# Kernel tuning notes

Measured on AMD Instinct MI355X. Metric: run time of the kernel, lower is better.

## Reference

```python
import jax, jax.numpy as jnp
import numpy as np

N_NODES = 8192
D = 7      # in_dim == out_dim (hardcoded 7x7 weight)
K = 32     # kNN fan-out


def setup_inputs() -> dict:
    key = jax.random.key(0)
    k1, k2, k3 = jax.random.split(key, 3)
    x = jax.random.normal(k1, (N_NODES, D + 1), dtype=jnp.float32)
    W = jax.random.normal(k2, (D, D), dtype=jnp.float32) * np.float32(1.0 / np.sqrt(D))
    a = jax.random.normal(k3, (2 * D,), dtype=jnp.float32) * np.float32(0.1)
    return {"x": x, "W": W, "a": a}


def _forward(x, W, a, k=K):
    # split pollutant channel (last column) from features, as in the torch forward
    pollutant = x[:, -1]          # (N,)
    feat = x[:, :-1]              # (N, D)
    N, d = feat.shape

    # linear transform (nn.functional.linear(x, weight) == x @ W.T)
    out = feat @ W.T              # (N, D)
    # nonlinearity_1 = Hardtanh
    out = jnp.clip(out, -1.0, 1.0)
    # (feature_weight = softmax(a) is computed in torch but unused for 'affine' kernel)

    # kNN graph built from input features (use_previous_graph=True).
    # Squared distances give the same neighbor ordering as euclidean norms.
    sq = jnp.sum(feat * feat, axis=1)                       # (N,)
    dist2 = sq[:, None] + sq[None, :] - 2.0 * (feat @ feat.T)
    dist2 = jnp.maximum(dist2, 0.0)
    dist2 = jnp.where(jnp.eye(N, dtype=bool), jnp.inf, dist2)  # dist[dist==0] = inf (self)
    _, nbr = jax.lax.top_k(-dist2, k)                       # (N, k) nearest neighbors

    out_n = out[nbr]                                        # (N, k, D) neighbor gather
    # affine attention: score_ij = concat(out_i, out_j) . a
    s = (out @ a[:d])[:, None] + out_n @ a[d:]              # (N, k)
    att = jax.nn.softmax(s, axis=-1)                        # per-node softmax over neighbors

    pol_n = pollutant[nbr]                                  # (N, k)
    xp = jnp.concatenate([out_n, pol_n[..., None]], axis=-1)  # (N, k, D+1)
    agg = jnp.einsum('nk,nkd->nd', att, xp)                 # attention-weighted aggregate

    y = jnp.concatenate([out, agg], axis=-1)                # (N, 2D+1)
    return y, att


def reference(x, W, a):
    y, att = _forward(x, W, a)
    # torch returns (y, y_, a) where y_ is y and a is the last node's attention row
    return (y, y, att[-1])
```

## Files before the change

### kernel.cpp

```cpp
#include <hip/hip_runtime.h>
#include <math.h>
#include <stdint.h>

#define N_NODES 8192
#define D 7
#define K 32
#define NT 512
#define QB 8
#define CPT (N_NODES / NT)
#define SUBC 8
#define ECAP2 256
#define DELTA 0.125f

typedef unsigned long long u64;
typedef _Float16 h2 __attribute__((ext_vector_type(2)));

__device__ __forceinline__ float rfl(float v) {
    return __uint_as_float(__builtin_amdgcn_readfirstlane(__float_as_uint(v)));
}
__device__ __forceinline__ unsigned rflu(unsigned v) {
    return __builtin_amdgcn_readfirstlane(v);
}
__device__ __forceinline__ h2 h2u(unsigned u) {
    union { unsigned u; h2 h; } t; t.u = u; return t.h;
}
__device__ __forceinline__ unsigned pkh(float a, float b) {
    union { h2 h; unsigned u; } t;
    t.h[0] = (_Float16)a; t.h[1] = (_Float16)b; return t.u;
}
__device__ __forceinline__ unsigned ordu(float f) {
    unsigned u = __float_as_uint(f);
    return (u & 0x80000000u) ? ~u : (u | 0x80000000u);
}
__device__ __forceinline__ float unordu(unsigned o) {
    unsigned u = (o & 0x80000000u) ? (o & 0x7fffffffu) : ~o;
    return __uint_as_float(u);
}

#if __has_builtin(__builtin_amdgcn_fdot2)
#define FDOT2(a, b, c) __builtin_amdgcn_fdot2((a), (b), (c), false)
#else
__device__ __forceinline__ float FDOT2(h2 a, h2 b, float c) {
    return fmaf((float)a[1], (float)b[1], fmaf((float)a[0], (float)b[0], c));
}
#endif

__device__ __forceinline__ float dist_m(float4 b0, float4 b1, float sqj,
                                        float4 A, float4 B) {
    float dot = A.x * b0.x;
    dot = fmaf(A.y, b0.y, dot);
    dot = fmaf(A.z, b0.z, dot);
    dot = fmaf(A.w, b0.w, dot);
    dot = fmaf(B.x, b1.x, dot);
    dot = fmaf(B.y, b1.y, dot);
    dot = fmaf(B.z, b1.z, dot);
    return fmaf(-2.0f, dot, sqj);
}

__device__ __forceinline__ float screen_m(uint4 dj, unsigned s0, unsigned s1,
                                          unsigned s2, unsigned s3) {
    return FDOT2(h2u(dj.x), h2u(s0),
           FDOT2(h2u(dj.y), h2u(s1),
           FDOT2(h2u(dj.z), h2u(s2),
           FDOT2(h2u(dj.w), h2u(s3), 0.f))));
}

__global__ __launch_bounds__(256)
void precompute_kernel(const float* __restrict__ x, const float* __restrict__ W,
                       float* __restrict__ outb, uint4* __restrict__ fh,
                       float4* __restrict__ xsq4)
{
    int n = blockIdx.x * 256 + threadIdx.x;
    float4 v0 = *reinterpret_cast<const float4*>(x + n * 8);
    float4 v1 = *reinterpret_cast<const float4*>(x + n * 8 + 4);
    float f[D] = {v0.x, v0.y, v0.z, v0.w, v1.x, v1.y, v1.z};
    float sq = 0.f;
#pragma unroll
    for (int c = 0; c < D; ++c) sq += f[c] * f[c];
    uint4 h;
    h.x = pkh(f[0], f[1]); h.y = pkh(f[2], f[3]);
    h.z = pkh(f[4], f[5]); h.w = pkh(f[6], sq);
    fh[n] = h;
    xsq4[n * 2]     = v0;
    xsq4[n * 2 + 1] = make_float4(v1.x, v1.y, v1.z, sq);
#pragma unroll
    for (int r = 0; r < D; ++r) {
        float acc = 0.f;
#pragma unroll
        for (int c = 0; c < D; ++c) acc += f[c] * W[r * D + c];
        acc = fminf(fmaxf(acc, -1.f), 1.f);
        outb[n * D + r] = acc;
    }
}

__global__ __launch_bounds__(NT, 4)
void gat_kernel(const float* __restrict__ x, const float* __restrict__ aw,
                const float* __restrict__ outb, const uint4* __restrict__ fh,
                const float4* __restrict__ xs4, float* __restrict__ dout)
{
    __shared__ u64      cand[QB][ECAP2];
    __shared__ int      nbr[QB][K];
    __shared__ unsigned selT[QB];
    __shared__ int      cnt2[QB];
    __shared__ float    redv[8];
    __shared__ int      redi[8];
    __shared__ float    bcv;
    __shared__ int      bci;

    float* Lmin = (float*)cand;

    const int tid  = threadIdx.x;
    const int lane = tid & 63;
    const int wave = tid >> 6;
    const int i0   = blockIdx.x * QB;

    unsigned qs0[QB], qs1[QB], qs2[QB], qs3[QB];
    float4 qA[QB], qBv[QB];
    float sqi[QB];
#pragma unroll
    for (int q = 0; q < QB; ++q) {
        const float* xq = x + (i0 + q) * 8;
        float4 a0 = *reinterpret_cast<const float4*>(xq);
        float4 a1 = *reinterpret_cast<const float4*>(xq + 4);
        float sq_ = rfl(xs4[(i0 + q) * 2 + 1].w);
        qs0[q] = rflu(pkh(-2.f * a0.x, -2.f * a0.y));
        qs1[q] = rflu(pkh(-2.f * a0.z, -2.f * a0.w));
        qs2[q] = rflu(pkh(-2.f * a1.x, -2.f * a1.y));
        qs3[q] = rflu(pkh(-2.f * a1.z, 1.0f));
        qA[q].x  = rfl(a0.x); qA[q].y  = rfl(a0.y);
        qA[q].z  = rfl(a0.z); qA[q].w  = rfl(a0.w);
        qBv[q].x = rfl(a1.x); qBv[q].y = rfl(a1.y);
        qBv[q].z = rfl(a1.z); qBv[q].w = sq_;
        sqi[q]   = sq_;
    }
    if (tid < QB) cnt2[tid] = 0;

    float lm[QB];
#pragma unroll
    for (int q = 0; q < QB; ++q) lm[q] = INFINITY;

#pragma unroll 4
    for (int c = 0; c < SUBC; ++c) {
        uint4 dj = fh[c * NT + tid];
#pragma unroll
        for (int q = 0; q < QB; ++q)
            lm[q] = fminf(lm[q], screen_m(dj, qs0[q], qs1[q], qs2[q], qs3[q]));
    }
#pragma unroll
    for (int q = 0; q < QB; ++q) Lmin[q * NT + tid] = lm[q];
    __syncthreads();

    {
        const int q = wave;
        unsigned ov0 = ordu(Lmin[q * NT +   0 + lane]);
        unsigned ov1 = ordu(Lmin[q * NT +  64 + lane]);
        unsigned ov2 = ordu(Lmin[q * NT + 128 + lane]);
        unsigned ov3 = ordu(Lmin[q * NT + 192 + lane]);
        unsigned ov4 = ordu(Lmin[q * NT + 256 + lane]);
        unsigned ov5 = ordu(Lmin[q * NT + 320 + lane]);
        unsigned ov6 = ordu(Lmin[q * NT + 384 + lane]);
        unsigned ov7 = ordu(Lmin[q * NT + 448 + lane]);
        unsigned lo = 0u, hi = 0xFFFFFFFFu;
        while (lo < hi) {
            unsigned mid = lo + ((hi - lo) >> 1);
            int cnt = __popcll(__ballot(ov0 <= mid))
                    + __popcll(__ballot(ov1 <= mid))
                    + __popcll(__ballot(ov2 <= mid))
                    + __popcll(__ballot(ov3 <= mid))
                    + __popcll(__ballot(ov4 <= mid))
                    + __popcll(__ballot(ov5 <= mid))
                    + __popcll(__ballot(ov6 <= mid))
                    + __popcll(__ballot(ov7 <= mid));
            if (cnt >= 34) hi = mid; else lo = mid + 1;
        }
        if (lane == 0) selT[q] = lo;
    }
    __syncthreads();

    float exq[QB];
#pragma unroll
    for (int q = 0; q < QB; ++q)
        exq[q] = fmaxf(unordu(selT[q]) + DELTA, -sqi[q]);

#pragma unroll 2
    for (int c = 0; c < CPT; ++c) {
        int j = c * NT + tid;
        float4 b0 = xs4[j * 2];
        float4 b1 = xs4[j * 2 + 1];
#pragma unroll
        for (int q = 0; q < QB; ++q) {
            float m = dist_m(b0, b1, b1.w, qA[q], qBv[q]);
            if (m <= exq[q] && j != i0 + q) {
                float d2c = fmaxf(sqi[q] + m, 0.f);
                u64 key = ((u64)__float_as_uint(d2c) << 32) | (unsigned)j;
                int p = atomicAdd(&cnt2[q], 1);
                if (p < ECAP2) cand[q][p] = key;
            }
        }
    }
    __syncthreads();

    {
        const int q = wave;
        const int M = cnt2[q];
        if (M >= K && M <= ECAP2) {
            for (int p = lane; p < M; p += 64) {
                u64 my = cand[q][p];
                int rank = 0;
                for (int m = 0; m < M; ++m)
                    rank += (cand[q][m] < my) ? 1 : 0;
                if (rank < K) nbr[q][rank] = (int)(my & 0xffffffffu);
            }
        }
    }
    __syncthreads();

#pragma unroll 1
    for (int q = 0; q < QB; ++q) {
        int M = cnt2[q];
        if (M < K || M > ECAP2) {
            const int iq = i0 + q;
            const float* xq = x + iq * 8;
            float4 A  = *reinterpret_cast<const float4*>(xq);
            float4 Bv = *reinterpret_cast<const float4*>(xq + 4);
            Bv.w = xs4[iq * 2 + 1].w;
            float lastv = -1.0f; int lasti = -1;
#pragma unroll 1
            for (int it = 0; it < K; ++it) {
                float best = INFINITY; int bidx = 0x7fffffff;
#pragma unroll 1
                for (int c = 0; c < CPT; ++c) {
                    int j = c * NT + tid;
                    float4 b0 = xs4[j * 2];
                    float4 b1 = xs4[j * 2 + 1];
                    float m = dist_m(b0, b1, b1.w, A, Bv);
                    float d2c = fmaxf(Bv.w + m, 0.f);
                    if (j == iq) continue;
                    bool gt = (d2c > lastv) || (d2c == lastv && j > lasti);
                    if (gt && (d2c < best || (d2c == best && j < bidx))) {
                        best = d2c; bidx = j;
                    }
                }
#pragma unroll
                for (int off = 32; off > 0; off >>= 1) {
                    float ov = __shfl_down(best, off);
                    int   oi = __shfl_down(bidx, off);
                    if (ov < best || (ov == best && oi < bidx)) { best = ov; bidx = oi; }
                }
                if (lane == 0) { redv[wave] = best; redi[wave] = bidx; }
                __syncthreads();
                if (tid == 0) {
                    float bv = redv[0]; int bi = redi[0];
#pragma unroll
                    for (int w = 1; w < 8; ++w)
                        if (redv[w] < bv || (redv[w] == bv && redi[w] < bi)) {
                            bv = redv[w]; bi = redi[w];
                        }
                    bcv = bv; bci = bi;
                    nbr[q][it] = bi;
                }
                __syncthreads();
                lastv = bcv; lasti = bci;
            }
        }
    }
    __syncthreads();

    {
        const int q  = wave;
        const int iq = i0 + q;
        if (lane < K) {
            int nk = nbr[q][lane];
            float s = 0.f;
#pragma unroll
            for (int c = 0; c < D; ++c) s += outb[iq * D + c] * aw[c];
            float xp[D + 1];
#pragma unroll
            for (int c = 0; c < D; ++c) {
                float on = outb[nk * D + c];
                xp[c] = on;
                s += on * aw[D + c];
            }
            xp[D] = x[nk * 8 + 7];

            float m = s;
#pragma unroll
            for (int off = 16; off > 0; off >>= 1) m = fmaxf(m, __shfl_xor(m, off, 32));
            float e = expf(s - m);
            float sum = e;
#pragma unroll
            for (int off = 16; off > 0; off >>= 1) sum += __shfl_xor(sum, off, 32);
            float att = e / sum;

            float agg[D + 1];
#pragma unroll
            for (int dd = 0; dd < D + 1; ++dd) {
                float v = att * xp[dd];
#pragma unroll
                for (int off = 16; off > 0; off >>= 1) v += __shfl_xor(v, off, 32);
                agg[dd] = v;
            }

            if (lane < D) {
                float o = outb[iq * D + lane];
                dout[iq * 15 + lane] = o;
                dout[N_NODES * 15 + iq * 15 + lane] = o;
            }
            if (lane < D + 1) {
                float av_ = agg[0];
#pragma unroll
                for (int dd = 1; dd < D + 1; ++dd) av_ = (lane == dd) ? agg[dd] : av_;
                dout[iq * 15 + D + lane] = av_;
                dout[N_NODES * 15 + iq * 15 + D + lane] = av_;
            }
            if (iq == N_NODES - 1) dout[2 * N_NODES * 15 + lane] = att;
        }
    }
}

extern "C" void kernel_launch(void* const* d_in, const int* in_sizes, int n_in,
                              void* d_out, int out_size, void* d_ws, size_t ws_size,
                              hipStream_t stream) {
    (void)in_sizes; (void)n_in; (void)out_size; (void)ws_size;
    const float* x = (const float*)d_in[0];
    const float* W = (const float*)d_in[1];
    const float* a = (const float*)d_in[2];
    float* out   = (float*)d_out;
    float* outb  = (float*)d_ws;
    uint4* fh    = (uint4*)(outb + N_NODES * D);
    float4* xsq4 = (float4*)(fh + N_NODES);

    hipLaunchKernelGGL(precompute_kernel, dim3(N_NODES / 256), dim3(256),
                       0, stream, x, W, outb, fh, xsq4);
    hipLaunchKernelGGL(gat_kernel, dim3(N_NODES / QB), dim3(NT),
                       0, stream, x, a, outb, fh, xsq4, out);
}
```

Measured before the change: 73.11 us.

## Use fp16 MFMA for kNN distance screening and a full-set candidate prefilter

Replaces the per-lane fdot2 screening over a subsample with 16x16x32 fp16 MFMA tiles over all nodes. The MFMA results feed both the per-tile minima used for threshold selection and a second screening pass that collects candidate indices into shared memory. The exact fp32 distance check then runs only on those candidates instead of scanning all 8192 nodes per query. This cuts the dense fp32 pass, but it adds a second full MFMA pass, shared-memory atomics, and fallback cases when the candidate list overflows.

```diff
diff --git a/kernel.cpp b/kernel.cpp
--- a/kernel.cpp
+++ b/kernel.cpp
@@ -8,21 +8,18 @@
 #define NT 512
 #define QB 8
 #define CPT (N_NODES / NT)
-#define SUBC 8
+#define SCAP 320
 #define ECAP2 256
 #define DELTA 0.125f
 
 typedef unsigned long long u64;
 typedef _Float16 h2 __attribute__((ext_vector_type(2)));
+typedef _Float16 f16x8 __attribute__((ext_vector_type(8)));
+typedef float f32x4 __attribute__((ext_vector_type(4)));
+union U4H8 { uint4 u; f16x8 h; };
 
 __device__ __forceinline__ float rfl(float v) {
     return __uint_as_float(__builtin_amdgcn_readfirstlane(__float_as_uint(v)));
-}
-__device__ __forceinline__ unsigned rflu(unsigned v) {
-    return __builtin_amdgcn_readfirstlane(v);
-}
-__device__ __forceinline__ h2 h2u(unsigned u) {
-    union { unsigned u; h2 h; } t; t.u = u; return t.h;
 }
 __device__ __forceinline__ unsigned pkh(float a, float b) {
     union { h2 h; unsigned u; } t;
@@ -36,14 +33,6 @@
     unsigned u = (o & 0x80000000u) ? (o & 0x7fffffffu) : ~o;
     return __uint_as_float(u);
 }
-
-#if __has_builtin(__builtin_amdgcn_fdot2)
-#define FDOT2(a, b, c) __builtin_amdgcn_fdot2((a), (b), (c), false)
-#else
-__device__ __forceinline__ float FDOT2(h2 a, h2 b, float c) {
-    return fmaf((float)a[1], (float)b[1], fmaf((float)a[0], (float)b[0], c));
-}
-#endif
 
 __device__ __forceinline__ float dist_m(float4 b0, float4 b1, float sqj,
                                         float4 A, float4 B) {
@@ -57,14 +46,6 @@
     return fmaf(-2.0f, dot, sqj);
 }
 
-__device__ __forceinline__ float screen_m(uint4 dj, unsigned s0, unsigned s1,
-                                          unsigned s2, unsigned s3) {
-    return FDOT2(h2u(dj.x), h2u(s0),
-           FDOT2(h2u(dj.y), h2u(s1),
-           FDOT2(h2u(dj.z), h2u(s2),
-           FDOT2(h2u(dj.w), h2u(s3), 0.f))));
-}
-
 __global__ __launch_bounds__(256)
 void precompute_kernel(const float* __restrict__ x, const float* __restrict__ W,
                        float* __restrict__ outb, uint4* __restrict__ fh,
@@ -99,8 +80,14 @@
                 const float4* __restrict__ xs4, float* __restrict__ dout)
 {
     __shared__ u64      cand[QB][ECAP2];
+    __shared__ unsigned short ent[QB][SCAP];
     __shared__ int      nbr[QB][K];
+    __shared__ uint4    qpk[16];
+    __shared__ float    sqfL[QB];
     __shared__ unsigned selT[QB];
+    __shared__ float    exqL[QB];
+    __shared__ float    scrL[16];
+    __shared__ int      scnt[QB];
     __shared__ int      cnt2[QB];
     __shared__ float    redv[8];
     __shared__ int      redi[8];
@@ -113,8 +100,9 @@
     const int lane = tid & 63;
     const int wave = tid >> 6;
     const int i0   = blockIdx.x * QB;
-
-    unsigned qs0[QB], qs1[QB], qs2[QB], qs3[QB];
+    const int col  = lane & 15;
+    const int lg   = lane >> 4;
+
     float4 qA[QB], qBv[QB];
     float sqi[QB];
 #pragma unroll
@@ -123,74 +111,116 @@
         float4 a0 = *reinterpret_cast<const float4*>(xq);
         float4 a1 = *reinterpret_cast<const float4*>(xq + 4);
         float sq_ = rfl(xs4[(i0 + q) * 2 + 1].w);
-        qs0[q] = rflu(pkh(-2.f * a0.x, -2.f * a0.y));
-        qs1[q] = rflu(pkh(-2.f * a0.z, -2.f * a0.w));
-        qs2[q] = rflu(pkh(-2.f * a1.x, -2.f * a1.y));
-        qs3[q] = rflu(pkh(-2.f * a1.z, 1.0f));
         qA[q].x  = rfl(a0.x); qA[q].y  = rfl(a0.y);
         qA[q].z  = rfl(a0.z); qA[q].w  = rfl(a0.w);
         qBv[q].x = rfl(a1.x); qBv[q].y = rfl(a1.y);
         qBv[q].z = rfl(a1.z); qBv[q].w = sq_;
         sqi[q]   = sq_;
     }
-    if (tid < QB) cnt2[tid] = 0;
-
-    float lm[QB];
-#pragma unroll
-    for (int q = 0; q < QB; ++q) lm[q] = INFINITY;
-
+    if (tid < 16) {
+        if (tid < QB) {
+            const float* xq = x + (i0 + tid) * 8;
+            float f0 = xq[0], f1 = xq[1], f2 = xq[2], f3 = xq[3];
+            float f4 = xq[4], f5 = xq[5], f6 = xq[6];
+            qpk[tid] = make_uint4(pkh(-2.f * f0, -2.f * f1),
+                                  pkh(-2.f * f2, -2.f * f3),
+                                  pkh(-2.f * f4, -2.f * f5),
+                                  pkh(-2.f * f6, 1.0f));
+            sqfL[tid] = f0*f0 + f1*f1 + f2*f2 + f3*f3 + f4*f4 + f5*f5 + f6*f6;
+            scnt[tid] = 0;
+            cnt2[tid] = 0;
+        } else {
+            qpk[tid] = make_uint4(0u, 0u, 0u, 0u);
+        }
+    }
+    __syncthreads();
+
+    U4H8 ub; ub.u = (lane < 16) ? qpk[lane] : make_uint4(0u, 0u, 0u, 0u);
+    const f16x8 bfrag = ub.h;
+    const f32x4 z4 = {0.f, 0.f, 0.f, 0.f};
+    const int tilebase = wave * 64;
+
+    float lm0 = INFINITY, lm1 = INFINITY, lm2 = INFINITY, lm3 = INFINITY;
 #pragma unroll 4
-    for (int c = 0; c < SUBC; ++c) {
-        uint4 dj = fh[c * NT + tid];
-#pragma unroll
-        for (int q = 0; q < QB; ++q)
-            lm[q] = fminf(lm[q], screen_m(dj, qs0[q], qs1[q], qs2[q], qs3[q]));
-    }
-#pragma unroll
-    for (int q = 0; q < QB; ++q) Lmin[q * NT + tid] = lm[q];
+    for (int tt = 0; tt < 64; ++tt) {
+        int t = tilebase + tt;
+        uint4 au = make_uint4(0u, 0u, 0u, 0u);
+        if (lane < 16) au = fh[t * 16 + lane];
+        U4H8 ua; ua.u = au;
+        f32x4 acc = __builtin_amdgcn_mfma_f32_16x16x32_f16(ua.h, bfrag, z4, 0, 0, 0);
+        lm0 = fminf(lm0, acc[0]);
+        lm1 = fminf(lm1, acc[1]);
+        lm2 = fminf(lm2, acc[2]);
+        lm3 = fminf(lm3, acc[3]);
+    }
+    {
+        int sb = wave * 16 + lg * 4;
+        Lmin[(sb + 0) * 16 + col] = lm0;
+        Lmin[(sb + 1) * 16 + col] = lm1;
+        Lmin[(sb + 2) * 16 + col] = lm2;
+        Lmin[(sb + 3) * 16 + col] = lm3;
+    }
     __syncthreads();
 
     {
         const int q = wave;
-        unsigned ov0 = ordu(Lmin[q * NT +   0 + lane]);
-        unsigned ov1 = ordu(Lmin[q * NT +  64 + lane]);
-        unsigned ov2 = ordu(Lmin[q * NT + 128 + lane]);
-        unsigned ov3 = ordu(Lmin[q * NT + 192 + lane]);
-        unsigned ov4 = ordu(Lmin[q * NT + 256 + lane]);
-        unsigned ov5 = ordu(Lmin[q * NT + 320 + lane]);
-        unsigned ov6 = ordu(Lmin[q * NT + 384 + lane]);
-        unsigned ov7 = ordu(Lmin[q * NT + 448 + lane]);
+        unsigned ov0 = ordu(Lmin[lane * 16 + q]);
+        unsigned ov1 = ordu(Lmin[(64 + lane) * 16 + q]);
         unsigned lo = 0u, hi = 0xFFFFFFFFu;
         while (lo < hi) {
             unsigned mid = lo + ((hi - lo) >> 1);
             int cnt = __popcll(__ballot(ov0 <= mid))
-                    + __popcll(__ballot(ov1 <= mid))
-                    + __popcll(__ballot(ov2 <= mid))
-                    + __popcll(__ballot(ov3 <= mid))
-                    + __popcll(__ballot(ov4 <= mid))
-                    + __popcll(__ballot(ov5 <= mid))
-                    + __popcll(__ballot(ov6 <= mid))
-                    + __popcll(__ballot(ov7 <= mid));
+                    + __popcll(__ballot(ov1 <= mid));
             if (cnt >= 34) hi = mid; else lo = mid + 1;
         }
         if (lane == 0) selT[q] = lo;
     }
     __syncthreads();
 
-    float exq[QB];
-#pragma unroll
-    for (int q = 0; q < QB; ++q)
-        exq[q] = fmaxf(unordu(selT[q]) + DELTA, -sqi[q]);
-
-#pragma unroll 2
-    for (int c = 0; c < CPT; ++c) {
-        int j = c * NT + tid;
-        float4 b0 = xs4[j * 2];
-        float4 b1 = xs4[j * 2 + 1];
-#pragma unroll
-        for (int q = 0; q < QB; ++q) {
+    if (tid < 16) {
+        if (tid < QB) {
+            float Ts = unordu(selT[tid]);
+            float sq_ = sqfL[tid];
+            exqL[tid] = fmaxf(Ts + DELTA, -sq_);
+            scrL[tid] = fmaxf(Ts + 2.f * DELTA, -sq_ + DELTA);
+        } else {
+            scrL[tid] = -INFINITY;
+        }
+    }
+    __syncthreads();
+
+    {
+        float myscr = scrL[col];
+#pragma unroll 4
+        for (int tt = 0; tt < 64; ++tt) {
+            int t = tilebase + tt;
+            uint4 au = make_uint4(0u, 0u, 0u, 0u);
+            if (lane < 16) au = fh[t * 16 + lane];
+            U4H8 ua; ua.u = au;
+            f32x4 acc = __builtin_amdgcn_mfma_f32_16x16x32_f16(ua.h, bfrag, z4, 0, 0, 0);
+#pragma unroll
+            for (int r = 0; r < 4; ++r) {
+                if (acc[r] <= myscr) {
+                    int j = t * 16 + lg * 4 + r;
+                    int p = atomicAdd(&scnt[col], 1);
+                    if (p < SCAP) ent[col][p] = (unsigned short)j;
+                }
+            }
+        }
+    }
+    __syncthreads();
+
+#pragma unroll
+    for (int q = 0; q < QB; ++q) {
+        int n = scnt[q];
+        if (n > SCAP) n = SCAP;
+        float thr = exqL[q];
+        for (int t = tid; t < n; t += NT) {
+            int j = ent[q][t];
+            float4 b0 = xs4[j * 2];
+            float4 b1 = xs4[j * 2 + 1];
             float m = dist_m(b0, b1, b1.w, qA[q], qBv[q]);
-            if (m <= exq[q] && j != i0 + q) {
+            if (m <= thr && j != i0 + q) {
                 float d2c = fmaxf(sqi[q] + m, 0.f);
                 u64 key = ((u64)__float_as_uint(d2c) << 32) | (unsigned)j;
                 int p = atomicAdd(&cnt2[q], 1);
@@ -203,7 +233,7 @@
     {
         const int q = wave;
         const int M = cnt2[q];
-        if (M >= K && M <= ECAP2) {
+        if (scnt[q] <= SCAP && M >= K && M <= ECAP2) {
             for (int p = lane; p < M; p += 64) {
                 u64 my = cand[q][p];
                 int rank = 0;
@@ -217,8 +247,9 @@
 
 #pragma unroll 1
     for (int q = 0; q < QB; ++q) {
+        int s = scnt[q];
         int M = cnt2[q];
-        if (M < K || M > ECAP2) {
+        if (s > SCAP || M < K || M > ECAP2) {
             const int iq = i0 + q;
             const float* xq = x + iq * 8;
             float4 A  = *reinterpret_cast<const float4*>(xq);
```

Measured after the change: 90.05 us. +23.2%, slower.
